# Kernel optimization log

Hardware: AMD Instinct MI355X
Metric: run time of the kernel (lower is better)

The kernel has to match this reference:

```python
import jax, jax.numpy as jnp
import numpy as np

N = 100000
C = 128
H = 8
D = C // H  # head_dim = 16
E = 640000


def setup_inputs() -> dict:
    key = jax.random.key(0)
    ks = jax.random.split(key, 10)
    s = 1.0 / np.sqrt(C)
    return {
        "features": jax.random.normal(ks[0], (N, C), dtype=jnp.float32),
        "edge_index": jax.random.randint(ks[1], (2, E), 0, N, dtype=jnp.int64),
        "Wq": jax.random.uniform(ks[2], (C, C), jnp.float32, -s, s),
        "bq": jnp.zeros((C,), jnp.float32),
        "Wk": jax.random.uniform(ks[3], (C, C), jnp.float32, -s, s),
        "bk": jnp.zeros((C,), jnp.float32),
        "Wv": jax.random.uniform(ks[4], (C, C), jnp.float32, -s, s),
        "bv": jnp.zeros((C,), jnp.float32),
        "Wo": jax.random.uniform(ks[5], (C, C), jnp.float32, -s, s),
        "bo": jnp.zeros((C,), jnp.float32),
    }


def reference(features, edge_index, Wq, bq, Wk, bk, Wv, bv, Wo, bo):
    row, col = edge_index[0], edge_index[1]  # [E], [E]
    # Linear projections (torch Linear: x @ W.T + b), reshape to heads
    q = (features @ Wq.T + bq).reshape(N, H, D)
    k = (features @ Wk.T + bk).reshape(N, H, D)
    v = (features @ Wv.T + bv).reshape(N, H, D)
    # Per-edge dot-product scores [E, H]
    attn = jnp.einsum('ehd,ehd->eh', q[row], k[col]) / jnp.sqrt(jnp.float32(D))
    # Faithful to original: softmax over ALL edges (dim=0), per head
    attn = jax.nn.softmax(attn, axis=0)
    # Weighted scatter-add of source values into destination nodes
    msgs = attn[:, :, None] * v[col]  # [E, H, D]
    out = jax.ops.segment_sum(msgs, row, num_segments=N)  # [N, H, D]
    out = out.reshape(N, C)
    return out @ Wo.T + bo
```

## Files before the change

kernel.cpp:

```cpp
#include <hip/hip_runtime.h>


#define TPB 256

typedef __attribute__((ext_vector_type(8))) short short8;
typedef __attribute__((ext_vector_type(4))) short short4v;
typedef __attribute__((ext_vector_type(4))) float f32x4;

__device__ __forceinline__ short f2bf(float f) {
    unsigned u = __float_as_uint(f);
    u += 0x7fffu + ((u >> 16) & 1u);
    return (short)(u >> 16);
}
__device__ __forceinline__ float bf2f(short s) {
    return __uint_as_float(((unsigned)(unsigned short)s) << 16);
}

__global__ void wconv_kernel(const float* __restrict__ W0, const float* __restrict__ W1,
                             const float* __restrict__ W2, const float* __restrict__ W3,
                             short* __restrict__ out)
{
    int i = blockIdx.x * TPB + threadIdx.x;
    if (i >= 65536) return;
    const float* W = (i < 16384) ? W0 : (i < 32768) ? W1 : (i < 49152) ? W2 : W3;
    out[i] = f2bf(W[i & 16383]);
}

template<bool IN_BF16, bool OUT_BF16>
__device__ __forceinline__ void gemm_body(
    const void* __restrict__ Xv, int nrows,
    const short* __restrict__ Wb, const float* __restrict__ bias,
    void* __restrict__ Yv)
{
    __shared__ short lw[16384];
    const int tid = threadIdx.x;

    #pragma unroll
    for (int r = 0; r < 8; ++r) {
        int c = r * 256 + tid;
        int fragid = c >> 6, ln = c & 63;
        int n = fragid >> 2, kc = fragid & 3;
        int row = n * 16 + (ln & 15);
        int col = kc * 32 + (ln >> 4) * 8;
        *(short8*)&lw[c * 8] = *(const short8*)&Wb[row * 128 + col];
    }
    __syncthreads();

    const int wid = tid >> 6;
    const int lane = tid & 63;
    const int l15 = lane & 15;
    const int lh  = lane >> 4;
    const int rowbase = blockIdx.x * 128 + wid * 32;

    f32x4 acc[8][2];
    #pragma unroll
    for (int n = 0; n < 8; ++n) { acc[n][0] = (f32x4)0.f; acc[n][1] = (f32x4)0.f; }

    const int r0 = rowbase + l15, r1 = r0 + 16;
    const bool v0 = r0 < nrows, v1 = r1 < nrows;

    #pragma unroll
    for (int kc = 0; kc < 4; ++kc) {
        short8 xf[2];
        if (IN_BF16) {
            const short* Xb = (const short*)Xv;
            xf[0] = v0 ? *(const short8*)&Xb[(size_t)r0 * 128 + kc*32 + lh*8]
                       : (short8)(short)0;
            xf[1] = v1 ? *(const short8*)&Xb[(size_t)r1 * 128 + kc*32 + lh*8]
                       : (short8)(short)0;
        } else {
            const float* Xf = (const float*)Xv;
            xf[0] = (short8)(short)0; xf[1] = (short8)(short)0;
            if (v0) {
                const float4* p = (const float4*)(Xf + (size_t)r0 * 128);
                float4 a = p[kc*8 + lh*2], b = p[kc*8 + lh*2 + 1];
                xf[0][0]=f2bf(a.x); xf[0][1]=f2bf(a.y); xf[0][2]=f2bf(a.z); xf[0][3]=f2bf(a.w);
                xf[0][4]=f2bf(b.x); xf[0][5]=f2bf(b.y); xf[0][6]=f2bf(b.z); xf[0][7]=f2bf(b.w);
            }
            if (v1) {
                const float4* p = (const float4*)(Xf + (size_t)r1 * 128);
                float4 a = p[kc*8 + lh*2], b = p[kc*8 + lh*2 + 1];
                xf[1][0]=f2bf(a.x); xf[1][1]=f2bf(a.y); xf[1][2]=f2bf(a.z); xf[1][3]=f2bf(a.w);
                xf[1][4]=f2bf(b.x); xf[1][5]=f2bf(b.y); xf[1][6]=f2bf(b.z); xf[1][7]=f2bf(b.w);
            }
        }
        short8 wf[8];
        #pragma unroll
        for (int n = 0; n < 8; ++n)
            wf[n] = *(const short8*)&lw[((n*4 + kc)*64 + lane) * 8];
        #pragma unroll
        for (int n = 0; n < 8; ++n) {
            acc[n][0] = __builtin_amdgcn_mfma_f32_16x16x32_bf16(wf[n], xf[0], acc[n][0], 0, 0, 0);
            acc[n][1] = __builtin_amdgcn_mfma_f32_16x16x32_bf16(wf[n], xf[1], acc[n][1], 0, 0, 0);
        }
    }

    #pragma unroll
    for (int g = 0; g < 2; ++g) {
        int row = rowbase + g*16 + l15;
        if (row >= nrows) continue;
        #pragma unroll
        for (int n = 0; n < 8; ++n) {
            float4 b4 = *(const float4*)&bias[n*16 + lh*4];
            float y0 = acc[n][g][0] + b4.x;
            float y1 = acc[n][g][1] + b4.y;
            float y2 = acc[n][g][2] + b4.z;
            float y3 = acc[n][g][3] + b4.w;
            if (OUT_BF16) {
                short4v s; s[0]=f2bf(y0); s[1]=f2bf(y1); s[2]=f2bf(y2); s[3]=f2bf(y3);
                *(short4v*)&((short*)Yv)[(size_t)row * 128 + n*16 + lh*4] = s;
            } else {
                *(float4*)&((float*)Yv)[(size_t)row * 128 + n*16 + lh*4] =
                    make_float4(y0, y1, y2, y3);
            }
        }
    }
}

__global__ __launch_bounds__(256) void gemm_out_kernel(
    const short* __restrict__ Xb, int nrows,
    const short* __restrict__ Wb, const float* __restrict__ bias,
    float* __restrict__ Y)
{
    gemm_body<true, false>(Xb, nrows, Wb, bias, Y);
}

__global__ __launch_bounds__(256) void gemm_qkv_kernel(
    const float* __restrict__ X, int nrows,
    const short* __restrict__ WB,
    const float* __restrict__ bq, const float* __restrict__ bk,
    const float* __restrict__ bv,
    short* __restrict__ Yb, size_t slice)
{
    int w = blockIdx.y;
    const float* bias = (w == 0) ? bq : (w == 1) ? bk : bv;
    gemm_body<false, true>(X, nrows, WB + w * 16384, bias, Yb + (size_t)w * slice);
}

__global__ void detect_i64_kernel(const int* __restrict__ raw, int* __restrict__ flag)
{
    if (blockIdx.x == 0 && threadIdx.x == 0) {
        int odd_nonzero = 0;
        for (int i = 0; i < 128; ++i)
            if (raw[2 * i + 1] != 0) odd_nonzero = 1;
        *flag = odd_nonzero ? 0 : 1;
    }
}

__global__ void conv_hist_kernel(const void* __restrict__ raw, int E,
                                 const int* __restrict__ flag,
                                 int* __restrict__ out, int* __restrict__ deg)
{
    int i = blockIdx.x * TPB + threadIdx.x;
    if (i >= 2 * E) return;
    int v;
    if (*flag) v = (int)((const long long*)raw)[i];
    else       v = ((const int*)raw)[i];
    out[i] = v;
    if (i < E) atomicAdd(&deg[v], 1);
}

__global__ void scan1_kernel(const int* __restrict__ deg, int n,
                             int* __restrict__ rowstart, int* __restrict__ bsum)
{
    __shared__ int sm[TPB];
    int t = threadIdx.x;
    int gid = blockIdx.x * TPB + t;
    int v = (gid < n) ? deg[gid] : 0;
    sm[t] = v;
    __syncthreads();
    for (int off = 1; off < TPB; off <<= 1) {
        int x = (t >= off) ? sm[t - off] : 0;
        __syncthreads();
        sm[t] += x;
        __syncthreads();
    }
    if (gid < n) rowstart[gid] = sm[t] - v;
    if (t == TPB - 1) bsum[blockIdx.x] = sm[t];
}

__global__ void scan2_kernel(int* __restrict__ bsum, int nb)
{
    __shared__ int sm[512];
    int t = threadIdx.x;
    int v = (t < nb) ? bsum[t] : 0;
    sm[t] = v;
    __syncthreads();
    for (int off = 1; off < 512; off <<= 1) {
        int x = (t >= off) ? sm[t - off] : 0;
        __syncthreads();
        sm[t] += x;
        __syncthreads();
    }
    if (t < nb) bsum[t] = sm[t] - v;
}

__global__ void scan3_kernel(int* __restrict__ rowstart, int* __restrict__ cursor,
                             int n, int E, const int* __restrict__ bsum)
{
    int gid = blockIdx.x * TPB + threadIdx.x;
    if (gid < n) {
        int v = rowstart[gid] + bsum[blockIdx.x];
        rowstart[gid] = v;
        cursor[gid] = v;
    }
    if (gid == 0) rowstart[n] = E;
}

__global__ void fill_kernel(const int* __restrict__ ei, int E,
                            int* __restrict__ cursor, int* __restrict__ ecol)
{
    int e = blockIdx.x * TPB + threadIdx.x;
    if (e >= E) return;
    int pos = atomicAdd(&cursor[ei[e]], 1);
    ecol[pos] = ei[E + e];
}

__global__ __launch_bounds__(256) void csr_score_stats_kernel(
    const short* __restrict__ Qb, const short* __restrict__ Kb,
    const int* __restrict__ ecol, const int* __restrict__ rowstart, int N,
    float* __restrict__ S, float* __restrict__ mpart, float* __restrict__ zpart)
{
    int t = threadIdx.x;
    int idx = blockIdx.x * TPB + t;
    float m = -3.0e38f, z = 0.f;
    if (idx < N * 8) {
        int node = idx >> 3, h = idx & 7;
        const short8* q8 = (const short8*)(Qb + (size_t)node * 128 + h * 16);
        short8 q0 = q8[0], q1 = q8[1];
        int p0 = rowstart[node], p1 = rowstart[node + 1];
        for (int p = p0; p < p1; ++p) {
            int c = ecol[p];
            const short8* k8 = (const short8*)(Kb + (size_t)c * 128 + h * 16);
            short8 k0 = k8[0], k1 = k8[1];
            float dot = 0.f;
            #pragma unroll
            for (int i = 0; i < 8; ++i) {
                dot += bf2f(q0[i]) * bf2f(k0[i]);
                dot += bf2f(q1[i]) * bf2f(k1[i]);
            }
            float s = dot * 0.25f;
            S[(size_t)p * 8 + h] = s;
            float M = fmaxf(m, s);
            z = z * __expf(m - M) + __expf(s - M);
            m = M;
        }
    }
    __shared__ float sm[TPB], sz[TPB];
    sm[t] = m; sz[t] = z;
    __syncthreads();
    for (int off = 128; off >= 8; off >>= 1) {
        if (t < off) {
            float m2 = sm[t + off], z2 = sz[t + off];
            float M = fmaxf(sm[t], m2);
            sz[t] = sz[t] * __expf(sm[t] - M) + z2 * __expf(m2 - M);
            sm[t] = M;
        }
        __syncthreads();
    }
    if (t < 8) {
        mpart[blockIdx.x * 8 + t] = sm[t];
        zpart[blockIdx.x * 8 + t] = sz[t];
    }
}

__global__ void stats_reduce_kernel(const float* __restrict__ mpart,
                                    const float* __restrict__ zpart,
                                    int nb, float* __restrict__ MZ)
{
    int t = threadIdx.x;
    int h = t & 7, chunk = t >> 3;
    float m = -3.0e38f, z = 0.f;
    for (int i = chunk; i < nb; i += 32) {
        float m2 = mpart[i * 8 + h], z2 = zpart[i * 8 + h];
        float M = fmaxf(m, m2);
        z = z * __expf(m - M) + z2 * __expf(m2 - M);
        m = M;
    }
    __shared__ float sm[TPB], sz[TPB];
    sm[t] = m; sz[t] = z;
    __syncthreads();
    for (int off = 128; off >= 8; off >>= 1) {
        if (t < off) {
            float m2 = sm[t + off], z2 = sz[t + off];
            float M = fmaxf(sm[t], m2);
            sz[t] = sz[t] * __expf(sm[t] - M) + z2 * __expf(m2 - M);
            sm[t] = M;
        }
        __syncthreads();
    }
    if (t < 8) { MZ[t] = sm[t]; MZ[8 + t] = sz[t]; }
}

__global__ __launch_bounds__(256) void gather_kernel(
    const float* __restrict__ S, const short* __restrict__ Vb,
    const int* __restrict__ ecol,
    const int* __restrict__ rowstart,
    const float* __restrict__ MZ, int N,
    short* __restrict__ outb)
{
    int idx = blockIdx.x * TPB + threadIdx.x;
    if (idx >= N * 8) return;
    int node = idx >> 3, h = idx & 7;
    float M = MZ[h];
    float invZ = 1.0f / MZ[8 + h];
    int p0 = rowstart[node], p1 = rowstart[node + 1];

    float a[16];
    #pragma unroll
    for (int i = 0; i < 16; ++i) a[i] = 0.f;

    for (int p = p0; p < p1; ++p) {
        int c = ecol[p];
        float w = __expf(S[(size_t)p * 8 + h] - M) * invZ;
        const short8* v8 = (const short8*)(Vb + (size_t)c * 128 + h * 16);
        short8 v0 = v8[0], v1 = v8[1];
        #pragma unroll
        for (int i = 0; i < 8; ++i) {
            a[i]     += w * bf2f(v0[i]);
            a[8 + i] += w * bf2f(v1[i]);
        }
    }
    short8 o0, o1;
    #pragma unroll
    for (int i = 0; i < 8; ++i) { o0[i] = f2bf(a[i]); o1[i] = f2bf(a[8 + i]); }
    short8* ob = (short8*)(outb + (size_t)node * 128 + h * 16);
    ob[0] = o0; ob[1] = o1;
}

extern "C" void kernel_launch(void* const* d_in, const int* in_sizes, int n_in,
                              void* d_out, int out_size, void* d_ws, size_t ws_size,
                              hipStream_t stream)
{
    const float* feat = (const float*)d_in[0];
    const void*  eraw = d_in[1];
    const float* Wq = (const float*)d_in[2];
    const float* bq = (const float*)d_in[3];
    const float* Wk = (const float*)d_in[4];
    const float* bk = (const float*)d_in[5];
    const float* Wv = (const float*)d_in[6];
    const float* bv = (const float*)d_in[7];
    const float* Wo = (const float*)d_in[8];
    const float* bo = (const float*)d_in[9];

    const int N = in_sizes[0] / 128;
    const int E = in_sizes[1] / 2;
    const size_t NC = (size_t)N * 128;
    const int EH = E * 8;
    const int gbN = (N * 8 + TPB - 1) / TPB;

    short* Qb   = (short*)d_ws;
    short* Kb   = Qb + NC;
    short* Vb   = Kb + NC;
    short* ACCb = Vb + NC;
    float* S    = (float*)(ACCb + NC);
    int*   EI   = (int*)(S + EH);
    short* WB   = (short*)(EI + 2 * E);
    float* mpart = (float*)(WB + 65536);
    float* zpart = mpart + (size_t)gbN * 8;
    float* MZ    = zpart + (size_t)gbN * 8;
    int*   flag  = (int*)(MZ + 16);
    int* deg      = flag + 16;
    int* rowstart = deg + N;
    int* cursor   = rowstart + N + 1;
    int* bsum     = cursor + N;
    int* ecol     = bsum + 512;

    const int nbS = (N + TPB - 1) / TPB;
    const int ebE = (E + TPB - 1) / TPB;

    hipMemsetAsync(deg, 0, (size_t)N * sizeof(int), stream);
    detect_i64_kernel<<<1, 64, 0, stream>>>((const int*)eraw, flag);
    conv_hist_kernel<<<(2 * E + TPB - 1) / TPB, TPB, 0, stream>>>(eraw, E, flag, EI, deg);
    scan1_kernel<<<nbS, TPB, 0, stream>>>(deg, N, rowstart, bsum);
    scan2_kernel<<<1, 512, 0, stream>>>(bsum, nbS);
    scan3_kernel<<<nbS, TPB, 0, stream>>>(rowstart, cursor, N, E, bsum);
    fill_kernel<<<ebE, TPB, 0, stream>>>(EI, E, cursor, ecol);

    wconv_kernel<<<256, TPB, 0, stream>>>(Wq, Wk, Wv, Wo, WB);
    const int gb = (N + 127) / 128;
    dim3 qkvgrid(gb, 3);
    gemm_qkv_kernel<<<qkvgrid, TPB, 0, stream>>>(feat, N, WB, bq, bk, bv, Qb, NC);

    csr_score_stats_kernel<<<gbN, TPB, 0, stream>>>(Qb, Kb, ecol, rowstart, N,
                                                    S, mpart, zpart);
    stats_reduce_kernel<<<1, TPB, 0, stream>>>(mpart, zpart, gbN, MZ);

    gather_kernel<<<gbN, TPB, 0, stream>>>(S, Vb, ecol, rowstart, MZ, N, ACCb);

    gemm_out_kernel<<<gb, TPB, 0, stream>>>(ACCb, N, WB + 3 * 16384, bo, (float*)d_out);
}
```

Baseline: 268.2 us.

## Prefetch GEMM inputs before LDS staging, remap QKV grid, software-pipeline edge loops

The GEMM body now loads weight and activation fragments into registers first and only then writes the weights to LDS, so global loads overlap instead of serialising behind the barrier. The QKV launch becomes a 1D grid interleaved so that consecutive blocks (spanning an 8-row-block group) cover all three projections of the same feature rows, aiming for L2 reuse of X. The score and gather loops software-prefetch the next edge's K/V row and score one iteration ahead to hide gather latency. This costs more registers, which may reduce occupancy.

```diff
diff --git a/kernel.cpp b/kernel.cpp
--- a/kernel.cpp
+++ b/kernel.cpp
@@ -30,68 +30,84 @@
 __device__ __forceinline__ void gemm_body(
     const void* __restrict__ Xv, int nrows,
     const short* __restrict__ Wb, const float* __restrict__ bias,
-    void* __restrict__ Yv)
+    void* __restrict__ Yv, int xblk)
 {
     __shared__ short lw[16384];
     const int tid = threadIdx.x;
 
+    short8 wreg[8];
     #pragma unroll
     for (int r = 0; r < 8; ++r) {
         int c = r * 256 + tid;
         int fragid = c >> 6, ln = c & 63;
         int n = fragid >> 2, kc = fragid & 3;
-        int row = n * 16 + (ln & 15);
-        int col = kc * 32 + (ln >> 4) * 8;
-        *(short8*)&lw[c * 8] = *(const short8*)&Wb[row * 128 + col];
-    }
-    __syncthreads();
+        wreg[r] = *(const short8*)&Wb[(n*16 + (ln & 15))*128 + kc*32 + (ln >> 4)*8];
+    }
 
     const int wid = tid >> 6;
     const int lane = tid & 63;
     const int l15 = lane & 15;
     const int lh  = lane >> 4;
-    const int rowbase = blockIdx.x * 128 + wid * 32;
+    const int rowbase = xblk * 128 + wid * 32;
+    const int r0 = rowbase + l15, r1 = r0 + 16;
+    const bool vv0 = r0 < nrows, vv1 = r1 < nrows;
+
+    short8 xfr[4][2];
+    if (IN_BF16) {
+        const short* Xb = (const short*)Xv;
+        #pragma unroll
+        for (int kc = 0; kc < 4; ++kc) {
+            xfr[kc][0] = vv0 ? *(const short8*)&Xb[(size_t)r0*128 + kc*32 + lh*8]
+                             : (short8)(short)0;
+            xfr[kc][1] = vv1 ? *(const short8*)&Xb[(size_t)r1*128 + kc*32 + lh*8]
+                             : (short8)(short)0;
+        }
+    } else {
+        const float* Xf = (const float*)Xv;
+        const float4* P0 = (const float4*)(Xf + (size_t)r0 * 128);
+        const float4* P1 = (const float4*)(Xf + (size_t)r1 * 128);
+        float4 xa[4][2], xb[4][2];
+        #pragma unroll
+        for (int kc = 0; kc < 4; ++kc) {
+            xa[kc][0] = vv0 ? P0[kc*8 + lh*2]     : make_float4(0.f,0.f,0.f,0.f);
+            xb[kc][0] = vv0 ? P0[kc*8 + lh*2 + 1] : make_float4(0.f,0.f,0.f,0.f);
+            xa[kc][1] = vv1 ? P1[kc*8 + lh*2]     : make_float4(0.f,0.f,0.f,0.f);
+            xb[kc][1] = vv1 ? P1[kc*8 + lh*2 + 1] : make_float4(0.f,0.f,0.f,0.f);
+        }
+        #pragma unroll
+        for (int kc = 0; kc < 4; ++kc)
+            #pragma unroll
+            for (int g = 0; g < 2; ++g) {
+                xfr[kc][g][0] = f2bf(xa[kc][g].x);
+                xfr[kc][g][1] = f2bf(xa[kc][g].y);
+                xfr[kc][g][2] = f2bf(xa[kc][g].z);
+                xfr[kc][g][3] = f2bf(xa[kc][g].w);
+                xfr[kc][g][4] = f2bf(xb[kc][g].x);
+                xfr[kc][g][5] = f2bf(xb[kc][g].y);
+                xfr[kc][g][6] = f2bf(xb[kc][g].z);
+                xfr[kc][g][7] = f2bf(xb[kc][g].w);
+            }
+    }
+
+    #pragma unroll
+    for (int r = 0; r < 8; ++r)
+        *(short8*)&lw[(r * 256 + tid) * 8] = wreg[r];
+    __syncthreads();
 
     f32x4 acc[8][2];
     #pragma unroll
     for (int n = 0; n < 8; ++n) { acc[n][0] = (f32x4)0.f; acc[n][1] = (f32x4)0.f; }
 
-    const int r0 = rowbase + l15, r1 = r0 + 16;
-    const bool v0 = r0 < nrows, v1 = r1 < nrows;
-
     #pragma unroll
     for (int kc = 0; kc < 4; ++kc) {
-        short8 xf[2];
-        if (IN_BF16) {
-            const short* Xb = (const short*)Xv;
-            xf[0] = v0 ? *(const short8*)&Xb[(size_t)r0 * 128 + kc*32 + lh*8]
-                       : (short8)(short)0;
-            xf[1] = v1 ? *(const short8*)&Xb[(size_t)r1 * 128 + kc*32 + lh*8]
-                       : (short8)(short)0;
-        } else {
-            const float* Xf = (const float*)Xv;
-            xf[0] = (short8)(short)0; xf[1] = (short8)(short)0;
-            if (v0) {
-                const float4* p = (const float4*)(Xf + (size_t)r0 * 128);
-                float4 a = p[kc*8 + lh*2], b = p[kc*8 + lh*2 + 1];
-                xf[0][0]=f2bf(a.x); xf[0][1]=f2bf(a.y); xf[0][2]=f2bf(a.z); xf[0][3]=f2bf(a.w);
-                xf[0][4]=f2bf(b.x); xf[0][5]=f2bf(b.y); xf[0][6]=f2bf(b.z); xf[0][7]=f2bf(b.w);
-            }
-            if (v1) {
-                const float4* p = (const float4*)(Xf + (size_t)r1 * 128);
-                float4 a = p[kc*8 + lh*2], b = p[kc*8 + lh*2 + 1];
-                xf[1][0]=f2bf(a.x); xf[1][1]=f2bf(a.y); xf[1][2]=f2bf(a.z); xf[1][3]=f2bf(a.w);
-                xf[1][4]=f2bf(b.x); xf[1][5]=f2bf(b.y); xf[1][6]=f2bf(b.z); xf[1][7]=f2bf(b.w);
-            }
-        }
         short8 wf[8];
         #pragma unroll
         for (int n = 0; n < 8; ++n)
             wf[n] = *(const short8*)&lw[((n*4 + kc)*64 + lane) * 8];
         #pragma unroll
         for (int n = 0; n < 8; ++n) {
-            acc[n][0] = __builtin_amdgcn_mfma_f32_16x16x32_bf16(wf[n], xf[0], acc[n][0], 0, 0, 0);
-            acc[n][1] = __builtin_amdgcn_mfma_f32_16x16x32_bf16(wf[n], xf[1], acc[n][1], 0, 0, 0);
+            acc[n][0] = __builtin_amdgcn_mfma_f32_16x16x32_bf16(wf[n], xfr[kc][0], acc[n][0], 0, 0, 0);
+            acc[n][1] = __builtin_amdgcn_mfma_f32_16x16x32_bf16(wf[n], xfr[kc][1], acc[n][1], 0, 0, 0);
         }
     }
 
@@ -122,19 +138,24 @@
     const short* __restrict__ Wb, const float* __restrict__ bias,
     float* __restrict__ Y)
 {
-    gemm_body<true, false>(Xb, nrows, Wb, bias, Y);
+    gemm_body<true, false>(Xb, nrows, Wb, bias, Y, blockIdx.x);
 }
 
 __global__ __launch_bounds__(256) void gemm_qkv_kernel(
-    const float* __restrict__ X, int nrows,
+    const float* __restrict__ X, int nrows, int nxblk,
     const short* __restrict__ WB,
     const float* __restrict__ bq, const float* __restrict__ bk,
     const float* __restrict__ bv,
     short* __restrict__ Yb, size_t slice)
 {
-    int w = blockIdx.y;
+    int b = blockIdx.x;
+    int k = b & 7, j = b >> 3;
+    int jd = j / 3, w = j - 3 * jd;
+    int x = k + 8 * jd;
+    if (x >= nxblk) return;
     const float* bias = (w == 0) ? bq : (w == 1) ? bk : bv;
-    gemm_body<false, true>(X, nrows, WB + w * 16384, bias, Yb + (size_t)w * slice);
+    gemm_body<false, true>(X, nrows, WB + w * 16384, bias,
+                           Yb + (size_t)w * slice, x);
 }
 
 __global__ void detect_i64_kernel(const int* __restrict__ raw, int* __restrict__ flag)
@@ -229,21 +250,28 @@
         const short8* q8 = (const short8*)(Qb + (size_t)node * 128 + h * 16);
         short8 q0 = q8[0], q1 = q8[1];
         int p0 = rowstart[node], p1 = rowstart[node + 1];
-        for (int p = p0; p < p1; ++p) {
-            int c = ecol[p];
-            const short8* k8 = (const short8*)(Kb + (size_t)c * 128 + h * 16);
-            short8 k0 = k8[0], k1 = k8[1];
-            float dot = 0.f;
-            #pragma unroll
-            for (int i = 0; i < 8; ++i) {
-                dot += bf2f(q0[i]) * bf2f(k0[i]);
-                dot += bf2f(q1[i]) * bf2f(k1[i]);
+        if (p0 < p1) {
+            const short8* kc = (const short8*)(Kb + (size_t)ecol[p0] * 128 + h * 16);
+            short8 k0 = kc[0], k1 = kc[1];
+            for (int p = p0; p < p1; ++p) {
+                short8 k0n = k0, k1n = k1;
+                if (p + 1 < p1) {
+                    const short8* kn = (const short8*)(Kb + (size_t)ecol[p+1] * 128 + h * 16);
+                    k0n = kn[0]; k1n = kn[1];
+                }
+                float dot = 0.f;
+                #pragma unroll
+                for (int i = 0; i < 8; ++i) {
+                    dot += bf2f(q0[i]) * bf2f(k0[i]);
+                    dot += bf2f(q1[i]) * bf2f(k1[i]);
+                }
+                float s = dot * 0.25f;
+                S[(size_t)p * 8 + h] = s;
+                float M = fmaxf(m, s);
+                z = z * __expf(m - M) + __expf(s - M);
+                m = M;
+                k0 = k0n; k1 = k1n;
             }
-            float s = dot * 0.25f;
-            S[(size_t)p * 8 + h] = s;
-            float M = fmaxf(m, s);
-            z = z * __expf(m - M) + __expf(s - M);
-            m = M;
         }
     }
     __shared__ float sm[TPB], sz[TPB];
@@ -310,15 +338,25 @@
     #pragma unroll
     for (int i = 0; i < 16; ++i) a[i] = 0.f;
 
-    for (int p = p0; p < p1; ++p) {
-        int c = ecol[p];
-        float w = __expf(S[(size_t)p * 8 + h] - M) * invZ;
-        const short8* v8 = (const short8*)(Vb + (size_t)c * 128 + h * 16);
-        short8 v0 = v8[0], v1 = v8[1];
-        #pragma unroll
-        for (int i = 0; i < 8; ++i) {
-            a[i]     += w * bf2f(v0[i]);
-            a[8 + i] += w * bf2f(v1[i]);
+    if (p0 < p1) {
+        const short8* vc = (const short8*)(Vb + (size_t)ecol[p0] * 128 + h * 16);
+        short8 v0 = vc[0], v1 = vc[1];
+        float sc = S[(size_t)p0 * 8 + h];
+        for (int p = p0; p < p1; ++p) {
+            short8 v0n = v0, v1n = v1;
+            float sn = sc;
+            if (p + 1 < p1) {
+                const short8* vn = (const short8*)(Vb + (size_t)ecol[p+1] * 128 + h * 16);
+                v0n = vn[0]; v1n = vn[1];
+                sn = S[(size_t)(p+1) * 8 + h];
+            }
+            float w = __expf(sc - M) * invZ;
+            #pragma unroll
+            for (int i = 0; i < 8; ++i) {
+                a[i]     += w * bf2f(v0[i]);
+                a[8 + i] += w * bf2f(v1[i]);
+            }
+            v0 = v0n; v1 = v1n; sc = sn;
         }
     }
     short8 o0, o1;
@@ -379,8 +417,8 @@
 
     wconv_kernel<<<256, TPB, 0, stream>>>(Wq, Wk, Wv, Wo, WB);
     const int gb = (N + 127) / 128;
-    dim3 qkvgrid(gb, 3);
-    gemm_qkv_kernel<<<qkvgrid, TPB, 0, stream>>>(feat, N, WB, bq, bk, bv, Qb, NC);
+    const int qkvgrid = 8 * 3 * ((gb + 7) / 8);
+    gemm_qkv_kernel<<<qkvgrid, TPB, 0, stream>>>(feat, N, gb, WB, bq, bk, bv, Qb, NC);
 
     csr_score_stats_kernel<<<gbN, TPB, 0, stream>>>(Qb, Kb, ecol, rowstart, N,
                                                     S, mpart, zpart);
```

New measurement: 259.3 us, median of 2. 3.3% less time.
